# Optimization experiments

Hardware: AMD Instinct MI355X
Metric: run time of the kernel (lower is better)

Reference implementation:

```python
import jax, jax.numpy as jnp
import numpy as np

B, N, C = 4, 2048, 1024
H = 16
HD = C // H  # head_dim = 64


def setup_inputs() -> dict:
    key = jax.random.key(0)
    k1, k2, k3 = jax.random.split(key, 3)
    x = jax.random.normal(k1, (B, N, C), dtype=jnp.float32)
    # nn.Linear-style init scale ~ 1/sqrt(fan_in)
    W_qkv = jax.random.normal(k2, (3 * C, C), dtype=jnp.float32) / np.sqrt(C)
    W_proj = jax.random.normal(k3, (C, C), dtype=jnp.float32) / np.sqrt(C)
    b_proj = jnp.zeros((C,), dtype=jnp.float32)
    return {"x": x, "W_qkv": W_qkv, "W_proj": W_proj, "b_proj": b_proj}


def reference(x, W_qkv, W_proj, b_proj):
    Bb, Nn, Cc = x.shape
    scale = (Cc // H) ** -0.5
    # qkv: [B,N,3C] -> [3,B,H,N,HD]
    qkv = jnp.einsum('bnc,dc->bnd', x, W_qkv)
    qkv = qkv.reshape(Bb, Nn, 3, H, Cc // H).transpose(2, 0, 3, 1, 4)
    q, k, v = qkv[0] * scale, qkv[1], qkv[2]
    attn = jnp.einsum('bhqd,bhkd->bhqk', q, k)  # [B,H,N,N]
    attn = jax.nn.softmax(attn, axis=-1)
    out = jnp.einsum('bhqk,bhkd->bhqd', attn, v)  # [B,H,N,HD]
    out = out.transpose(0, 2, 1, 3).reshape(Bb, Nn, Cc)
    return jnp.einsum('bnc,dc->bnd', out, W_proj) + b_proj
```

## Files before the change

kernel.cpp:

```cpp
#include <hip/hip_runtime.h>

typedef _Float16 f16;
typedef _Float16 half8 __attribute__((ext_vector_type(8)));
typedef _Float16 half4 __attribute__((ext_vector_type(4)));
typedef __fp16 fp16x2 __attribute__((ext_vector_type(2)));
typedef float float4_ __attribute__((ext_vector_type(4)));
typedef float f32x16 __attribute__((ext_vector_type(16)));
typedef unsigned int uint2_ __attribute__((ext_vector_type(2)));

#define MFMA16(a, b, c) __builtin_amdgcn_mfma_f32_16x16x32_f16(a, b, c, 0, 0, 0)
#define MFMA32(a, b, c) __builtin_amdgcn_mfma_f32_32x32x16_f16(a, b, c, 0, 0, 0)

__device__ __forceinline__ void gld_lds16(const void* g, void* l) {
    __builtin_amdgcn_global_load_lds(
        (const __attribute__((address_space(1))) void*)g,
        (__attribute__((address_space(3))) void*)l, 16, 0, 0);
}

__device__ __forceinline__ unsigned pkrtz(float a, float b) {
    union { fp16x2 h; unsigned u; } c;
    c.h = __builtin_amdgcn_cvt_pkrtz(a, b);
    return c.u;
}

__global__ void cast_kernel(const float* __restrict__ in, f16* __restrict__ out,
                            int n, int qboundary, float qscale) {
    int i = (blockIdx.x * blockDim.x + threadIdx.x) * 4;
    if (i >= n) return;
    float4_ v = *(const float4_*)(in + i);
    float sc = (i < qboundary) ? qscale : 1.0f;
    half4 h;
    h[0] = (f16)(v[0] * sc);
    h[1] = (f16)(v[1] * sc);
    h[2] = (f16)(v[2] * sc);
    h[3] = (f16)(v[3] * sc);
    *(half4*)(out + i) = h;
}

__global__ __launch_bounds__(256, 2)
void qkv_gemm(const f16* __restrict__ X, const f16* __restrict__ W,
              f16* __restrict__ Q, f16* __restrict__ Kq, f16* __restrict__ V) {
    const int K = 1024;
    __shared__ __align__(16) f16 sA[128 * 64];
    __shared__ __align__(16) f16 sB[128 * 64];
    int tid = threadIdx.x;
    int lane = tid & 63, wave = tid >> 6;
    int wm = wave >> 1, wn = wave & 1;
    int l15 = lane & 15, quad = lane >> 4;
    int rowBase = blockIdx.y * 128;
    int colBase = blockIdx.x * 128;

    float4_ acc[4][4] = {};

    for (int k0 = 0; k0 < K; k0 += 64) {
        for (int i = 0; i < 4; ++i) {
            int seg = wave * 4 + i;
            int e = (seg * 64 + lane) * 8;
            int r = e >> 6, c = e & 63;
            gld_lds16(X + (size_t)(rowBase + r) * K + k0 + c, sA + seg * 512);
            gld_lds16(W + (size_t)(colBase + r) * K + k0 + c, sB + seg * 512);
        }
        __syncthreads();
        for (int ks = 0; ks < 2; ++ks) {
            half8 a[4], b[4];
            for (int mt = 0; mt < 4; ++mt)
                a[mt] = *(const half8*)&sA[(wm * 64 + mt * 16 + l15) * 64 + ks * 32 + quad * 8];
            for (int nt = 0; nt < 4; ++nt)
                b[nt] = *(const half8*)&sB[(wn * 64 + nt * 16 + l15) * 64 + ks * 32 + quad * 8];
            for (int mt = 0; mt < 4; ++mt)
                for (int nt = 0; nt < 4; ++nt)
                    acc[mt][nt] = MFMA16(a[mt], b[nt], acc[mt][nt]);
        }
        __syncthreads();
    }

    for (int mt = 0; mt < 4; ++mt) {
        int m0 = rowBase + wm * 64 + mt * 16 + quad * 4;
        for (int nt = 0; nt < 4; ++nt) {
            int d = colBase + wn * 64 + nt * 16 + l15;
            int part = d >> 10;
            int h = (d >> 6) & 15;
            int hd = d & 63;
            f16* dst = (part == 0) ? Q : (part == 1) ? Kq : V;
            for (int r = 0; r < 4; ++r) {
                int m = m0 + r;
                int b = m >> 11, n = m & 2047;
                dst[(size_t)((b * 16 + h) * 2048 + n) * 64 + hd] = (f16)acc[mt][nt][r];
            }
        }
    }
}

__global__ __launch_bounds__(256, 2)
void attn_kernel(const f16* __restrict__ Q, const f16* __restrict__ Kk,
                 const f16* __restrict__ V, f16* __restrict__ O) {
    const int bh = blockIdx.y;
    const int qt = blockIdx.x;
    const f16* Qb = Q + (size_t)bh * 2048 * 64;
    const f16* Kb = Kk + (size_t)bh * 2048 * 64;
    const f16* Vb = V + (size_t)bh * 2048 * 64;
    int tid = threadIdx.x, lane = tid & 63, wave = tid >> 6;
    int l31 = lane & 31, hi = lane >> 5;

    __shared__ __align__(16) f16 Vt[2][64 * 72];

    int qbase = qt * 128 + wave * 32;

    half8 aQ[4];
#pragma unroll
    for (int d = 0; d < 4; ++d)
        aQ[d] = *(const half8*)(Qb + (size_t)(qbase + l31) * 64 + d * 16 + hi * 8);

    f32x16 oacc0 = {}, oacc1 = {}, lacc = {};
    float mrow = -1e30f;

    half8 vone;
#pragma unroll
    for (int j = 0; j < 8; ++j) vone[j] = (f16)1.0f;

    half8 bK0[4], bK1[4];
#pragma unroll
    for (int d = 0; d < 4; ++d) {
        bK0[d] = *(const half8*)(Kb + (size_t)(l31) * 64 + d * 16 + hi * 8);
        bK1[d] = *(const half8*)(Kb + (size_t)(32 + l31) * 64 + d * 16 + hi * 8);
    }
    {
        const f16* vsrc = Vb + (size_t)lane * 64 + wave * 16;
        half8 v0 = *(const half8*)(vsrc);
        half8 v1 = *(const half8*)(vsrc + 8);
#pragma unroll
        for (int j = 0; j < 8; ++j) {
            Vt[0][(wave * 16 + j) * 72 + lane] = v0[j];
            Vt[0][(wave * 16 + 8 + j) * 72 + lane] = v1[j];
        }
    }

#pragma unroll 2
    for (int it = 0; it < 32; ++it) {
        int buf = it & 1;
        __syncthreads();

        f32x16 s0 = {}, s1 = {};
#pragma unroll
        for (int d = 0; d < 4; ++d) s0 = MFMA32(bK0[d], aQ[d], s0);
#pragma unroll
        for (int d = 0; d < 4; ++d) s1 = MFMA32(bK1[d], aQ[d], s1);

        half8 bK0n[4], bK1n[4], v0n, v1n;
        if (it < 31) {
            int t1 = (it + 1) * 64;
#pragma unroll
            for (int d = 0; d < 4; ++d) {
                bK0n[d] = *(const half8*)(Kb + (size_t)(t1 + l31) * 64 + d * 16 + hi * 8);
                bK1n[d] = *(const half8*)(Kb + (size_t)(t1 + 32 + l31) * 64 + d * 16 + hi * 8);
            }
            const f16* vsrc = Vb + (size_t)(t1 + lane) * 64 + wave * 16;
            v0n = *(const half8*)(vsrc);
            v1n = *(const half8*)(vsrc + 8);
        }

        float mx = s0[0];
#pragma unroll
        for (int r = 1; r < 16; ++r) mx = fmaxf(mx, s0[r]);
#pragma unroll
        for (int r = 0; r < 16; ++r) mx = fmaxf(mx, s1[r]);
        mx = fmaxf(mx, __shfl_xor(mx, 32, 64));

        if (__any(mx > mrow + 8.0f)) {
            float mnew = fmaxf(mrow, mx);
            float alpha = exp2f(mrow - mnew);
            mrow = mnew;
#pragma unroll
            for (int r = 0; r < 16; ++r) {
                int cr = (r & 3) + 8 * (r >> 2) + 4 * hi;
                float ar = __shfl(alpha, cr, 64);
                oacc0[r] *= ar;
                oacc1[r] *= ar;
                lacc[r] *= ar;
            }
        }

#pragma unroll
        for (int r = 0; r < 16; ++r) s0[r] = exp2f(s0[r] - mrow);
#pragma unroll
        for (int r = 0; r < 16; ++r) s1[r] = exp2f(s1[r] - mrow);

        half8 PA[4];
        {
            union { half8 h; unsigned u[4]; } w;
            uint2_ r02 = __builtin_amdgcn_permlane32_swap(pkrtz(s0[0], s0[1]), pkrtz(s0[4], s0[5]), false, false);
            uint2_ r13 = __builtin_amdgcn_permlane32_swap(pkrtz(s0[2], s0[3]), pkrtz(s0[6], s0[7]), false, false);
            w.u[0] = r02[0]; w.u[1] = r13[0]; w.u[2] = r02[1]; w.u[3] = r13[1];
            PA[0] = w.h;
            r02 = __builtin_amdgcn_permlane32_swap(pkrtz(s0[8], s0[9]), pkrtz(s0[12], s0[13]), false, false);
            r13 = __builtin_amdgcn_permlane32_swap(pkrtz(s0[10], s0[11]), pkrtz(s0[14], s0[15]), false, false);
            w.u[0] = r02[0]; w.u[1] = r13[0]; w.u[2] = r02[1]; w.u[3] = r13[1];
            PA[1] = w.h;
            r02 = __builtin_amdgcn_permlane32_swap(pkrtz(s1[0], s1[1]), pkrtz(s1[4], s1[5]), false, false);
            r13 = __builtin_amdgcn_permlane32_swap(pkrtz(s1[2], s1[3]), pkrtz(s1[6], s1[7]), false, false);
            w.u[0] = r02[0]; w.u[1] = r13[0]; w.u[2] = r02[1]; w.u[3] = r13[1];
            PA[2] = w.h;
            r02 = __builtin_amdgcn_permlane32_swap(pkrtz(s1[8], s1[9]), pkrtz(s1[12], s1[13]), false, false);
            r13 = __builtin_amdgcn_permlane32_swap(pkrtz(s1[10], s1[11]), pkrtz(s1[14], s1[15]), false, false);
            w.u[0] = r02[0]; w.u[1] = r13[0]; w.u[2] = r02[1]; w.u[3] = r13[1];
            PA[3] = w.h;
        }

#pragma unroll
        for (int ks = 0; ks < 4; ++ks) {
            half8 vf0 = *(const half8*)&Vt[buf][(l31) * 72 + ks * 16 + hi * 8];
            half8 vf1 = *(const half8*)&Vt[buf][(32 + l31) * 72 + ks * 16 + hi * 8];
            oacc0 = MFMA32(PA[ks], vf0, oacc0);
            oacc1 = MFMA32(PA[ks], vf1, oacc1);
            lacc = MFMA32(PA[ks], vone, lacc);
        }

        if (it < 31) {
#pragma unroll
            for (int j = 0; j < 8; ++j) {
                Vt[buf ^ 1][(wave * 16 + j) * 72 + lane] = v0n[j];
                Vt[buf ^ 1][(wave * 16 + 8 + j) * 72 + lane] = v1n[j];
            }
#pragma unroll
            for (int d = 0; d < 4; ++d) {
                bK0[d] = bK0n[d];
                bK1[d] = bK1n[d];
            }
        }
    }

    int b = bh >> 4, h = bh & 15;
#pragma unroll
    for (int r = 0; r < 16; ++r) {
        int cr = (r & 3) + 8 * (r >> 2) + 4 * hi;
        int n = qbase + cr;
        float inv = 1.0f / lacc[r];
        O[(size_t)(b * 2048 + n) * 1024 + h * 64 + l31] = (f16)(oacc0[r] * inv);
        O[(size_t)(b * 2048 + n) * 1024 + h * 64 + 32 + l31] = (f16)(oacc1[r] * inv);
    }
}

__global__ __launch_bounds__(256, 2)
void proj_gemm(const f16* __restrict__ A, const f16* __restrict__ W,
               const float* __restrict__ bias, float* __restrict__ out) {
    const int K = 1024;
    __shared__ __align__(16) f16 sA[128 * 64];
    __shared__ __align__(16) f16 sB[128 * 64];
    int tid = threadIdx.x;
    int lane = tid & 63, wave = tid >> 6;
    int wm = wave >> 1, wn = wave & 1;
    int l15 = lane & 15, quad = lane >> 4;
    int rowBase = blockIdx.y * 128;
    int colBase = blockIdx.x * 128;

    float4_ acc[4][4] = {};

    for (int k0 = 0; k0 < K; k0 += 64) {
        for (int i = 0; i < 4; ++i) {
            int seg = wave * 4 + i;
            int e = (seg * 64 + lane) * 8;
            int r = e >> 6, c = e & 63;
            gld_lds16(A + (size_t)(rowBase + r) * K + k0 + c, sA + seg * 512);
            gld_lds16(W + (size_t)(colBase + r) * K + k0 + c, sB + seg * 512);
        }
        __syncthreads();
        for (int ks = 0; ks < 2; ++ks) {
            half8 a[4], b[4];
            for (int mt = 0; mt < 4; ++mt)
                a[mt] = *(const half8*)&sA[(wm * 64 + mt * 16 + l15) * 64 + ks * 32 + quad * 8];
            for (int nt = 0; nt < 4; ++nt)
                b[nt] = *(const half8*)&sB[(wn * 64 + nt * 16 + l15) * 64 + ks * 32 + quad * 8];
            for (int mt = 0; mt < 4; ++mt)
                for (int nt = 0; nt < 4; ++nt)
                    acc[mt][nt] = MFMA16(a[mt], b[nt], acc[mt][nt]);
        }
        __syncthreads();
    }

    for (int mt = 0; mt < 4; ++mt) {
        int m0 = rowBase + wm * 64 + mt * 16 + quad * 4;
        for (int nt = 0; nt < 4; ++nt) {
            int d = colBase + wn * 64 + nt * 16 + l15;
            float bv = bias[d];
            for (int r = 0; r < 4; ++r) {
                int m = m0 + r;
                out[(size_t)m * 1024 + d] = acc[mt][nt][r] + bv;
            }
        }
    }
}

extern "C" void kernel_launch(void* const* d_in, const int* in_sizes, int n_in,
                              void* d_out, int out_size, void* d_ws, size_t ws_size,
                              hipStream_t stream) {
    const float* x     = (const float*)d_in[0];
    const float* Wqkv  = (const float*)d_in[1];
    const float* Wproj = (const float*)d_in[2];
    const float* bproj = (const float*)d_in[3];
    float* out = (float*)d_out;

    f16* ws     = (f16*)d_ws;
    f16* xb     = ws;
    f16* wqkvb  = xb + 8388608;
    f16* wprojb = wqkvb + 3145728;
    f16* q      = wprojb + 1048576;
    f16* k      = q + 8388608;
    f16* v      = k + 8388608;
    f16* ao     = v + 8388608;

    const float qscale = 0.125f * 1.4426950408889634f;

    cast_kernel<<<8192, 256, 0, stream>>>(x, xb, 8388608, 0, 1.f);
    cast_kernel<<<3072, 256, 0, stream>>>(Wqkv, wqkvb, 3145728, 1048576, qscale);
    cast_kernel<<<1024, 256, 0, stream>>>(Wproj, wprojb, 1048576, 0, 1.f);

    qkv_gemm<<<dim3(24, 64), 256, 0, stream>>>(xb, wqkvb, q, k, v);
    attn_kernel<<<dim3(16, 64), 256, 0, stream>>>(q, k, v, ao);
    proj_gemm<<<dim3(8, 64), 256, 0, stream>>>(ao, wprojb, bproj, out);
}
```

Measured before the change: 343.3 us.

## Raise attention occupancy, remap block order, add MFMA priority and max3 reduction

Changes the attention kernel's launch bounds from 2 to 4 blocks per CU, which forces lower register use and may cause spills. It remaps the linear block index so consecutive blocks spread across different batch-heads. It raises wave priority around the MFMA sections with s_setprio so waves interleave better, and replaces the serial fmax row-max chain with a v_max3 tree. The changes are independent tuning ideas applied together, and the register cap is the main risk.

```diff
diff --git a/kernel.cpp b/kernel.cpp
--- a/kernel.cpp
+++ b/kernel.cpp
@@ -21,6 +21,12 @@
     union { fp16x2 h; unsigned u; } c;
     c.h = __builtin_amdgcn_cvt_pkrtz(a, b);
     return c.u;
+}
+
+__device__ __forceinline__ float max3f(float a, float b, float c) {
+    float d;
+    asm("v_max3_f32 %0, %1, %2, %3" : "=v"(d) : "v"(a), "v"(b), "v"(c));
+    return d;
 }
 
 __global__ void cast_kernel(const float* __restrict__ in, f16* __restrict__ out,
@@ -91,11 +97,13 @@
     }
 }
 
-__global__ __launch_bounds__(256, 2)
+__global__ __launch_bounds__(256, 4)
 void attn_kernel(const f16* __restrict__ Q, const f16* __restrict__ Kk,
                  const f16* __restrict__ V, f16* __restrict__ O) {
-    const int bh = blockIdx.y;
-    const int qt = blockIdx.x;
+    int L = blockIdx.y * gridDim.x + blockIdx.x;
+    int m_ = L & 63;
+    int bh = (m_ & 7) * 8 + (m_ >> 3);
+    int qt = L >> 6;
     const f16* Qb = Q + (size_t)bh * 2048 * 64;
     const f16* Kb = Kk + (size_t)bh * 2048 * 64;
     const f16* Vb = V + (size_t)bh * 2048 * 64;
@@ -141,10 +149,12 @@
         __syncthreads();
 
         f32x16 s0 = {}, s1 = {};
+        __builtin_amdgcn_s_setprio(1);
 #pragma unroll
         for (int d = 0; d < 4; ++d) s0 = MFMA32(bK0[d], aQ[d], s0);
 #pragma unroll
         for (int d = 0; d < 4; ++d) s1 = MFMA32(bK1[d], aQ[d], s1);
+        __builtin_amdgcn_s_setprio(0);
 
         half8 bK0n[4], bK1n[4], v0n, v1n;
         if (it < 31) {
@@ -159,11 +169,22 @@
             v1n = *(const half8*)(vsrc + 8);
         }
 
-        float mx = s0[0];
-#pragma unroll
-        for (int r = 1; r < 16; ++r) mx = fmaxf(mx, s0[r]);
-#pragma unroll
-        for (int r = 0; r < 16; ++r) mx = fmaxf(mx, s1[r]);
+        float a0 = max3f(s0[0], s0[1], s0[2]);
+        float a1 = max3f(s0[3], s0[4], s0[5]);
+        float a2 = max3f(s0[6], s0[7], s0[8]);
+        float a3 = max3f(s0[9], s0[10], s0[11]);
+        float a4 = max3f(s0[12], s0[13], s0[14]);
+        float a5 = max3f(s0[15], s1[0], s1[1]);
+        float a6 = max3f(s1[2], s1[3], s1[4]);
+        float a7 = max3f(s1[5], s1[6], s1[7]);
+        float a8 = max3f(s1[8], s1[9], s1[10]);
+        float a9 = max3f(s1[11], s1[12], s1[13]);
+        float a10 = fmaxf(s1[14], s1[15]);
+        float b0 = max3f(a0, a1, a2);
+        float b1 = max3f(a3, a4, a5);
+        float b2 = max3f(a6, a7, a8);
+        float b3 = fmaxf(a9, a10);
+        float mx = fmaxf(max3f(b0, b1, b2), b3);
         mx = fmaxf(mx, __shfl_xor(mx, 32, 64));
 
         if (__any(mx > mrow + 8.0f)) {
@@ -206,6 +227,7 @@
             PA[3] = w.h;
         }
 
+        __builtin_amdgcn_s_setprio(1);
 #pragma unroll
         for (int ks = 0; ks < 4; ++ks) {
             half8 vf0 = *(const half8*)&Vt[buf][(l31) * 72 + ks * 16 + hi * 8];
@@ -214,6 +236,7 @@
             oacc1 = MFMA32(PA[ks], vf1, oacc1);
             lacc = MFMA32(PA[ks], vone, lacc);
         }
+        __builtin_amdgcn_s_setprio(0);
 
         if (it < 31) {
 #pragma unroll
```

After: 643.6 us. +87.4%, slower.
